# Kernel optimization log

Measured on AMD Instinct MI355X. Metric: run time of the kernel, lower is better.

The kernel has to match this reference:

```python
import jax, jax.numpy as jnp
import numpy as np

TEMPERATURE = 0.07

def _l2norm(x):
    return x / jnp.linalg.norm(x, axis=-1, keepdims=True)

def setup_inputs() -> dict:
    key = jax.random.key(0)
    k1, k2, k3, k4 = jax.random.split(key, 4)
    B, T, C_ctx, C_enc, P, K = 8, 256, 512, 256, 12, 128
    context = jax.random.normal(k1, (B, T, C_ctx), dtype=jnp.float32)
    encoded = jax.random.normal(k2, (B, T, C_enc), dtype=jnp.float32)
    W = jax.random.normal(k3, (P, C_enc, C_ctx), dtype=jnp.float32) * (1.0 / np.sqrt(C_ctx))
    neg_idx = jax.random.randint(k4, (P, B * (T - 1), K), 0, B * T, dtype=jnp.int64)
    return {"context": context, "encoded": encoded, "W": W, "neg_idx": neg_idx}

def reference(context, encoded, W, neg_idx):
    B, T, C_enc = encoded.shape
    n_pred = W.shape[0]
    # normalized pool of all encoded vectors [B*T, C_enc]
    pool = _l2norm(encoded.reshape(B * T, C_enc))
    total = jnp.float32(0.0)
    for k in range(1, n_pred + 1):  # fixed small loop over horizons
        Nk = B * (T - k)
        c_t = context[:, : T - k, :]                       # [B, T-k, C_ctx]
        z_hat = jnp.einsum('btc,ec->bte', c_t, W[k - 1])   # [B, T-k, C_enc]
        z_hat = _l2norm(z_hat.reshape(Nk, C_enc))
        z_pos = _l2norm(encoded[:, k:, :].reshape(Nk, C_enc))
        pos_logits = jnp.sum(z_hat * z_pos, axis=-1, keepdims=True)  # [Nk, 1]
        z_neg = pool[neg_idx[k - 1, :Nk]]                  # [Nk, K, C_enc]
        neg_logits = jnp.einsum('nc,nkc->nk', z_hat, z_neg)
        logits = jnp.concatenate([pos_logits, neg_logits], axis=1) / TEMPERATURE
        # cross-entropy with target class 0
        step_loss = jnp.mean(jax.nn.logsumexp(logits, axis=-1) - logits[:, 0])
        total = total + step_loss
    return total / n_pred
```

## Files before the change

### kernel.cpp

```cpp
#include <hip/hip_runtime.h>
#include <hip/hip_bf16.h>

typedef __attribute__((ext_vector_type(8))) short short8;
typedef __attribute__((ext_vector_type(4))) float f32x4;
typedef _Float16 __attribute__((ext_vector_type(2))) half2v;

#define INV_TEMP 14.285714285714286f
#define LOGIT_MAX 14.2857143f
#define L2E 1.44269504f
#define OFFE (LOGIT_MAX * L2E)

__device__ __forceinline__ ushort bf16c(float f) {
  uint u = __float_as_uint(f);
  uint r = (u + 0x7fffu + ((u >> 16) & 1u)) >> 16;
  return (ushort)r;
}
__device__ __forceinline__ uint pk2(float a, float b) {
  return (uint)bf16c(a) | ((uint)bf16c(b) << 16);
}
__device__ __forceinline__ uint pkh(float a, float b) {
  return __builtin_bit_cast(uint, __builtin_amdgcn_cvt_pkrtz(a, b));
}
__device__ __forceinline__ half2v h2(uint u) {
  return __builtin_bit_cast(half2v, u);
}
__device__ __forceinline__ float fdot2(half2v a, half2v b, float c) {
  return __builtin_amdgcn_fdot2(a, b, c, false);
}
__device__ __forceinline__ int sdot4_(uint a, uint b, int c) {
  return __builtin_amdgcn_sdot4((int)a, (int)b, c, false);
}

template <int CTRL>
__device__ __forceinline__ float dpp_add(float v) {
  const int x = __builtin_amdgcn_mov_dpp(__float_as_int(v), CTRL, 0xF, 0xF, true);
  return v + __int_as_float(x);
}
template <int CTRL>
__device__ __forceinline__ int dpp_addi(int v) {
  return v + __builtin_amdgcn_mov_dpp(v, CTRL, 0xF, 0xF, true);
}
__device__ __forceinline__ float qsum16(float v) {
  v = dpp_add<0xB1>(v);
  v = dpp_add<0x4E>(v);
  v = dpp_add<0x141>(v);
  v = dpp_add<0x140>(v);
  return v;
}
__device__ __forceinline__ int qsum8i(int v) {
  v = dpp_addi<0xB1>(v);
  v = dpp_addi<0x4E>(v);
  v = dpp_addi<0x141>(v);
  return v;
}

__global__ __launch_bounds__(256) void cvt_bf16_kernel(
    const float* __restrict__ in, ushort* __restrict__ out) {
  const int i = blockIdx.x * 256 + threadIdx.x;
  const float4 a = *(const float4*)(in + (size_t)i * 8);
  const float4 b = *(const float4*)(in + (size_t)i * 8 + 4);
  const uint4 o = make_uint4(pk2(a.x, a.y), pk2(a.z, a.w), pk2(b.x, b.y), pk2(b.z, b.w));
  *(uint4*)(out + (size_t)i * 8) = o;
}

__global__ __launch_bounds__(256) void pool_norm_kernel(
    const float* __restrict__ enc, uint* __restrict__ pool8) {
  const int tid = threadIdx.x;
  const int grp = tid >> 4, lane = tid & 15;
  const int r = blockIdx.x * 16 + grp;
  const float* src = enc + (size_t)r * 256 + lane * 16;
  float4 v0 = *(const float4*)(src);
  float4 v1 = *(const float4*)(src + 4);
  float4 v2 = *(const float4*)(src + 8);
  float4 v3 = *(const float4*)(src + 12);
  float c[16] = {v0.x, v0.y, v0.z, v0.w, v1.x, v1.y, v1.z, v1.w,
                 v2.x, v2.y, v2.z, v2.w, v3.x, v3.y, v3.z, v3.w};
  float ss = 0.f;
#pragma unroll
  for (int i = 0; i < 16; ++i) ss = fmaf(c[i], c[i], ss);
  ss = qsum16(ss);
  const float s127 = rsqrtf(ss) * 127.f;
  uint q[4];
#pragma unroll
  for (int i = 0; i < 4; ++i) {
    const int a = (int)rintf(c[4 * i] * s127);
    const int b = (int)rintf(c[4 * i + 1] * s127);
    const int cc = (int)rintf(c[4 * i + 2] * s127);
    const int d = (int)rintf(c[4 * i + 3] * s127);
    q[i] = (a & 255) | ((b & 255) << 8) | ((cc & 255) << 16) | ((uint)d << 24);
  }
  *(uint4*)(pool8 + (size_t)r * 64 + lane * 4) = make_uint4(q[0], q[1], q[2], q[3]);
}

__global__ __launch_bounds__(256) void zhat_gemm_kernel(
    const ushort* __restrict__ ctxb, const ushort* __restrict__ Wb,
    uint* __restrict__ Zp) {
  const int kk = blockIdx.z;
  const int Tk = 255 - kk, Nk = 8 * Tk;
  const int rowbase = blockIdx.y * 64;
  if (rowbase >= Nk) return;
  const int colbase = blockIdx.x * 128;

  __shared__ ushort As[64 * 40];
  __shared__ ushort Bs[128 * 40];

  const int tid = threadIdx.x;
  const int arow = tid & 63;
  const int akseg = (tid >> 6) * 8;
  int n = rowbase + arow;
  if (n >= Nk) n = Nk - 1;
  const int bb = n / Tk, tt = n - bb * Tk;
  const ushort* aptr = ctxb + ((size_t)(bb * 256 + tt)) * 512 + akseg;
  const int brow = tid & 127;
  const int bk0 = (tid >> 7) * 8;
  const ushort* bptr = Wb + ((size_t)kk * 256 + colbase + brow) * 512 + bk0;

  const int wid = tid >> 6, lane = tid & 63;
  const int wm = wid >> 1, wn = wid & 1;
  const int l15 = lane & 15, l16 = lane >> 4;

  f32x4 acc[2][4];
#pragma unroll
  for (int i = 0; i < 2; ++i)
#pragma unroll
    for (int j = 0; j < 4; ++j) acc[i][j] = (f32x4){0.f, 0.f, 0.f, 0.f};

  const ushort* aread = &As[(wm * 32 + l15) * 40 + l16 * 8];
  const ushort* bread = &Bs[(wn * 64 + l15) * 40 + l16 * 8];

  for (int k0 = 0; k0 < 512; k0 += 32) {
    const uint4 av = *(const uint4*)(aptr + k0);
    const uint4 bv0 = *(const uint4*)(bptr + k0);
    const uint4 bv1 = *(const uint4*)(bptr + k0 + 16);
    __syncthreads();
    *(uint4*)&As[arow * 40 + akseg] = av;
    *(uint4*)&Bs[brow * 40 + bk0] = bv0;
    *(uint4*)&Bs[brow * 40 + bk0 + 16] = bv1;
    __syncthreads();
    short8 bf[4];
#pragma unroll
    for (int nb = 0; nb < 4; ++nb) bf[nb] = *(const short8*)(bread + nb * 16 * 40);
#pragma unroll
    for (int mb = 0; mb < 2; ++mb) {
      short8 af = *(const short8*)(aread + mb * 16 * 40);
#pragma unroll
      for (int nb = 0; nb < 4; ++nb)
        acc[mb][nb] = __builtin_amdgcn_mfma_f32_16x16x32_bf16(af, bf[nb], acc[mb][nb], 0, 0, 0);
    }
  }

#pragma unroll
  for (int mb = 0; mb < 2; ++mb) {
    const int row0 = rowbase + wm * 32 + mb * 16 + l16 * 4;
#pragma unroll
    for (int r = 0; r < 4; ++r) {
      const int row = row0 + r;
      if (row < Nk) {
        uint* zp = Zp + ((size_t)kk * 2040 + row) * 128 + (colbase >> 1) + wn * 32 + l15;
        zp[0]  = pkh(acc[mb][0][r], acc[mb][1][r]);
        zp[16] = pkh(acc[mb][2][r], acc[mb][3][r]);
      }
    }
  }
}

__device__ __forceinline__ int dot32_i8(const uint* __restrict__ zq,
                                        const uint4 p0, const uint4 p1) {
  int d0 = 0, d1 = 0;
  d0 = sdot4_(zq[0], p0.x, d0); d1 = sdot4_(zq[1], p0.y, d1);
  d0 = sdot4_(zq[2], p0.z, d0); d1 = sdot4_(zq[3], p0.w, d1);
  d0 = sdot4_(zq[4], p1.x, d0); d1 = sdot4_(zq[5], p1.y, d1);
  d0 = sdot4_(zq[6], p1.z, d0); d1 = sdot4_(zq[7], p1.w, d1);
  return d0 + d1;
}

#define LDB(P, IDX) { const uint* p_ = pbase + (size_t)(uint)(IDX) * 64;        \
    P##0 = *(const uint4*)p_; P##1 = *(const uint4*)(p_ + 4); }
#define ACCB(S, P)                                                              \
  S += exp2f(fmaf((float)qsum8i(dot32_i8(zq, P##0, P##1)), sceq, -OFFE));

__global__ __launch_bounds__(256) void loss_kernel(
    const uint* __restrict__ Zp, const uint* __restrict__ pool8,
    const int* __restrict__ neg_idx, float* __restrict__ acc) {
  const int kk = blockIdx.y;
  const int Tk = 255 - kk, Nk = 8 * Tk;
  if ((int)(blockIdx.x * 32) >= Nk) return;
  const int tid = threadIdx.x;
  const int n = blockIdx.x * 32 + (tid >> 3);
  const int g = tid & 7;
  float row_loss = 0.f;
  if (n < Nk) {
    const uint* zr = Zp + ((size_t)kk * 2040 + n) * 128 + g * 16;
    uint zu[16];
#pragma unroll
    for (int i = 0; i < 4; ++i) *(uint4*)(zu + 4 * i) = *(const uint4*)(zr + 4 * i);
    float ss = 0.f;
#pragma unroll
    for (int i = 0; i < 16; ++i) {
      const half2v h = h2(zu[i]);
      ss = fdot2(h, h, ss);
    }
    ss = dpp_add<0xB1>(ss); ss = dpp_add<0x4E>(ss); ss = dpp_add<0x141>(ss);
    const float s127 = rsqrtf(ss) * 127.f;
    uint zq[8];
#pragma unroll
    for (int t = 0; t < 8; ++t) {
      float e0, e1, e2, e3;
      if (t < 4) {
        e0 = (float)h2(zu[4 * t]).x;     e1 = (float)h2(zu[4 * t + 1]).x;
        e2 = (float)h2(zu[4 * t + 2]).x; e3 = (float)h2(zu[4 * t + 3]).x;
      } else {
        e0 = (float)h2(zu[4 * t - 16]).y; e1 = (float)h2(zu[4 * t - 15]).y;
        e2 = (float)h2(zu[4 * t - 14]).y; e3 = (float)h2(zu[4 * t - 13]).y;
      }
      const int a = (int)rintf(e0 * s127), b = (int)rintf(e1 * s127);
      const int c = (int)rintf(e2 * s127), d = (int)rintf(e3 * s127);
      zq[t] = (a & 255) | ((b & 255) << 8) | ((c & 255) << 16) | ((uint)d << 24);
    }
    int nq = 0;
#pragma unroll
    for (int t = 0; t < 8; ++t) nq = sdot4_(zq[t], zq[t], nq);
    nq = qsum8i(nq);
    const float sceq = (INV_TEMP * L2E) / (sqrtf((float)nq) * 127.f);

    const uint* pbase = pool8 + g * 8;
    const int bb = n / Tk, tt = n - bb * Tk;
    uint4 A0, A1, B0, B1, C0, C1, D0, D1, E0, E1, F0, F1, G0, G1, H0, H1;
    LDB(A, bb * 256 + tt + kk + 1)
    const float pose = (float)qsum8i(dot32_i8(zq, A0, A1)) * sceq;

    const int* ip = neg_idx + ((size_t)kk * 2040 + n) * 128;
    float s0 = 0.f, s1 = 0.f, s2 = 0.f, s3 = 0.f;
    {
      const int4 iv = *(const int4*)ip;
      LDB(A, iv.x) LDB(B, iv.y) LDB(C, iv.z) LDB(D, iv.w)
    }
    for (int j8 = 0; j8 < 16; ++j8) {
      {
        const int4 jv = *(const int4*)(ip + j8 * 8 + 4);
        LDB(E, jv.x) LDB(F, jv.y) LDB(G, jv.z) LDB(H, jv.w)
      }
      ACCB(s0, A) ACCB(s1, B) ACCB(s2, C) ACCB(s3, D)
      if (j8 < 15) {
        const int4 kv = *(const int4*)(ip + j8 * 8 + 8);
        LDB(A, kv.x) LDB(B, kv.y) LDB(C, kv.z) LDB(D, kv.w)
      }
      ACCB(s0, E) ACCB(s1, F) ACCB(s2, G) ACCB(s3, H)
    }
    const float ssum = (s0 + s1) + (s2 + s3) + exp2f(pose - OFFE);
    row_loss = LOGIT_MAX + 0.69314718f * (__log2f(ssum) - pose);
  }
  const float v = dpp_add<0x140>(row_loss);
  __shared__ float bl[16];
  if ((tid & 15) == 0) bl[tid >> 4] = v;
  __syncthreads();
  if (tid == 0) {
    float s = 0.f;
#pragma unroll
    for (int i = 0; i < 16; ++i) s += bl[i];
    atomicAdd(&acc[kk], s);
  }
}

__global__ void finalize_kernel(const float* __restrict__ acc,
                                float* __restrict__ out) {
  if (threadIdx.x == 0) {
    float tot = 0.f;
#pragma unroll
    for (int kk = 0; kk < 12; ++kk) tot += acc[kk] / (8.0f * (255 - kk));
    out[0] = tot / 12.0f;
  }
}

extern "C" void kernel_launch(void* const* d_in, const int* in_sizes, int n_in,
                              void* d_out, int out_size, void* d_ws, size_t ws_size,
                              hipStream_t stream) {
  const float* ctx = (const float*)d_in[0];
  const float* enc = (const float*)d_in[1];
  const float* W   = (const float*)d_in[2];
  const int*   neg = (const int*)d_in[3];
  float* out = (float*)d_out;

  char* ws = (char*)d_ws;
  uint*   pool8 = (uint*)(ws);
  ushort* ctxb  = (ushort*)(ws + 524288);
  ushort* Wb    = (ushort*)(ws + 2621440);
  uint*   Zp    = (uint*)(ws + 5767168);
  float*  acc   = (float*)(ws + 5767168 + 12533760);

  hipMemsetAsync(acc, 0, 12 * sizeof(float), stream);
  cvt_bf16_kernel<<<dim3(512), dim3(256), 0, stream>>>(ctx, ctxb);
  cvt_bf16_kernel<<<dim3(768), dim3(256), 0, stream>>>(W, Wb);
  pool_norm_kernel<<<dim3(128), dim3(256), 0, stream>>>(enc, pool8);
  zhat_gemm_kernel<<<dim3(2, 32, 12), dim3(256), 0, stream>>>(ctxb, Wb, Zp);
  loss_kernel<<<dim3(64, 12), dim3(256), 0, stream>>>(Zp, pool8, neg, acc);
  finalize_kernel<<<dim3(1), dim3(64), 0, stream>>>(acc, out);
}
```

Measured before the change: 74.53 us.

## Split loss rows across 16 lanes, merge cvt launches, fold acc memset

The loss kernel now gives each row 16 lanes instead of 8. Each half of the lanes handles 64 of the 128 negatives, and the two halves are combined with a DPP add. The grid doubles, which raises parallelism and memory-level concurrency for the latency-bound gather. The two bf16 conversion launches are merged into one, and the accumulator memset moves into pool_norm_kernel, removing launch overhead. The per-row normalisation and quantisation work is now duplicated across both halves.

```diff
diff --git a/kernel.cpp b/kernel.cpp
--- a/kernel.cpp
+++ b/kernel.cpp
@@ -55,17 +55,25 @@
 }
 
 __global__ __launch_bounds__(256) void cvt_bf16_kernel(
-    const float* __restrict__ in, ushort* __restrict__ out) {
-  const int i = blockIdx.x * 256 + threadIdx.x;
-  const float4 a = *(const float4*)(in + (size_t)i * 8);
-  const float4 b = *(const float4*)(in + (size_t)i * 8 + 4);
+    const float* __restrict__ ctx, const float* __restrict__ W,
+    ushort* __restrict__ ctxb, ushort* __restrict__ Wb) {
+  const int bid = blockIdx.x;
+  const float* in;
+  ushort* out;
+  size_t i;
+  if (bid < 512) { in = ctx; out = ctxb; i = (size_t)bid * 256 + threadIdx.x; }
+  else           { in = W;   out = Wb;   i = (size_t)(bid - 512) * 256 + threadIdx.x; }
+  const float4 a = *(const float4*)(in + i * 8);
+  const float4 b = *(const float4*)(in + i * 8 + 4);
   const uint4 o = make_uint4(pk2(a.x, a.y), pk2(a.z, a.w), pk2(b.x, b.y), pk2(b.z, b.w));
-  *(uint4*)(out + (size_t)i * 8) = o;
+  *(uint4*)(out + i * 8) = o;
 }
 
 __global__ __launch_bounds__(256) void pool_norm_kernel(
-    const float* __restrict__ enc, uint* __restrict__ pool8) {
+    const float* __restrict__ enc, uint* __restrict__ pool8,
+    float* __restrict__ acc) {
   const int tid = threadIdx.x;
+  if (blockIdx.x == 0 && tid < 12) acc[tid] = 0.f;
   const int grp = tid >> 4, lane = tid & 15;
   const int r = blockIdx.x * 16 + grp;
   const float* src = enc + (size_t)r * 256 + lane * 16;
@@ -184,10 +192,12 @@
     const int* __restrict__ neg_idx, float* __restrict__ acc) {
   const int kk = blockIdx.y;
   const int Tk = 255 - kk, Nk = 8 * Tk;
-  if ((int)(blockIdx.x * 32) >= Nk) return;
+  if ((int)(blockIdx.x * 16) >= Nk) return;
   const int tid = threadIdx.x;
-  const int n = blockIdx.x * 32 + (tid >> 3);
-  const int g = tid & 7;
+  const int n = blockIdx.x * 16 + (tid >> 4);
+  const int l = tid & 15;
+  const int h = l >> 3;
+  const int g = l & 7;
   float row_loss = 0.f;
   if (n < Nk) {
     const uint* zr = Zp + ((size_t)kk * 2040 + n) * 128 + g * 16;
@@ -197,8 +207,8 @@
     float ss = 0.f;
 #pragma unroll
     for (int i = 0; i < 16; ++i) {
-      const half2v h = h2(zu[i]);
-      ss = fdot2(h, h, ss);
+      const half2v hv = h2(zu[i]);
+      ss = fdot2(hv, hv, ss);
     }
     ss = dpp_add<0xB1>(ss); ss = dpp_add<0x4E>(ss); ss = dpp_add<0x141>(ss);
     const float s127 = rsqrtf(ss) * 127.f;
@@ -229,30 +239,31 @@
     LDB(A, bb * 256 + tt + kk + 1)
     const float pose = (float)qsum8i(dot32_i8(zq, A0, A1)) * sceq;
 
-    const int* ip = neg_idx + ((size_t)kk * 2040 + n) * 128;
+    const int* ip = neg_idx + ((size_t)kk * 2040 + n) * 128 + h * 64;
     float s0 = 0.f, s1 = 0.f, s2 = 0.f, s3 = 0.f;
     {
       const int4 iv = *(const int4*)ip;
       LDB(A, iv.x) LDB(B, iv.y) LDB(C, iv.z) LDB(D, iv.w)
     }
-    for (int j8 = 0; j8 < 16; ++j8) {
+    for (int j8 = 0; j8 < 8; ++j8) {
       {
         const int4 jv = *(const int4*)(ip + j8 * 8 + 4);
         LDB(E, jv.x) LDB(F, jv.y) LDB(G, jv.z) LDB(H, jv.w)
       }
       ACCB(s0, A) ACCB(s1, B) ACCB(s2, C) ACCB(s3, D)
-      if (j8 < 15) {
+      if (j8 < 7) {
         const int4 kv = *(const int4*)(ip + j8 * 8 + 8);
         LDB(A, kv.x) LDB(B, kv.y) LDB(C, kv.z) LDB(D, kv.w)
       }
       ACCB(s0, E) ACCB(s1, F) ACCB(s2, G) ACCB(s3, H)
     }
-    const float ssum = (s0 + s1) + (s2 + s3) + exp2f(pose - OFFE);
+    float sl = (s0 + s1) + (s2 + s3);
+    sl = dpp_add<0x140>(sl);
+    const float ssum = sl + exp2f(pose - OFFE);
     row_loss = LOGIT_MAX + 0.69314718f * (__log2f(ssum) - pose);
   }
-  const float v = dpp_add<0x140>(row_loss);
   __shared__ float bl[16];
-  if ((tid & 15) == 0) bl[tid >> 4] = v;
+  if (l == 0) bl[tid >> 4] = row_loss;
   __syncthreads();
   if (tid == 0) {
     float s = 0.f;
@@ -288,11 +299,9 @@
   uint*   Zp    = (uint*)(ws + 5767168);
   float*  acc   = (float*)(ws + 5767168 + 12533760);
 
-  hipMemsetAsync(acc, 0, 12 * sizeof(float), stream);
-  cvt_bf16_kernel<<<dim3(512), dim3(256), 0, stream>>>(ctx, ctxb);
-  cvt_bf16_kernel<<<dim3(768), dim3(256), 0, stream>>>(W, Wb);
-  pool_norm_kernel<<<dim3(128), dim3(256), 0, stream>>>(enc, pool8);
+  cvt_bf16_kernel<<<dim3(1280), dim3(256), 0, stream>>>(ctx, W, ctxb, Wb);
+  pool_norm_kernel<<<dim3(128), dim3(256), 0, stream>>>(enc, pool8, acc);
   zhat_gemm_kernel<<<dim3(2, 32, 12), dim3(256), 0, stream>>>(ctxb, Wb, Zp);
-  loss_kernel<<<dim3(64, 12), dim3(256), 0, stream>>>(Zp, pool8, neg, acc);
+  loss_kernel<<<dim3(128, 12), dim3(256), 0, stream>>>(Zp, pool8, neg, acc);
   finalize_kernel<<<dim3(1), dim3(64), 0, stream>>>(acc, out);
 }
```

Result: faster. 70.17 us (-5.9%).
